# Performance work log

Measured on AMD Instinct MI355X. Metric: run time of the kernel, lower is better.

Reference implementation:

```python
import jax, jax.numpy as jnp
import numpy as np

DIM = 64
K = 7
GC = 8            # groups_channels (hardcoded in module)
G = DIM // GC     # groups = 8
RED = 2           # reduction_ratio
PAD = (K - 1) // 2


def _patches(y, k, p):
    # torch nn.Unfold(k, dilation=1, padding=p, stride=1) ordering: (c, kh, kw)
    b, c, H, W = y.shape
    yp = jnp.pad(y, ((0, 0), (0, 0), (p, p), (p, p)))
    tiles = [yp[:, :, i:i + H, j:j + W] for i in range(k) for j in range(k)]
    return jnp.stack(tiles, axis=2)  # (b, c, k*k, H, W)


def setup_inputs() -> dict:
    key = jax.random.key(0)
    ks = jax.random.split(key, 6)
    b, h, w = 4, 128, 128
    input_x = jax.random.normal(ks[0], (b, DIM, h, w), dtype=jnp.float32)
    input_y = jax.random.normal(ks[1], (b, DIM, h, w), dtype=jnp.float32)
    c_mid = DIM // RED
    w1 = jax.random.normal(ks[2], (c_mid, DIM), dtype=jnp.float32) * 0.05
    b1 = jnp.zeros((c_mid,), dtype=jnp.float32)
    w2 = jax.random.normal(ks[3], (K * K * G, c_mid), dtype=jnp.float32) * 0.05
    b2 = jnp.zeros((K * K * G,), dtype=jnp.float32)
    return {"input_x": input_x, "input_y": input_y, "w1": w1, "b1": b1, "w2": w2, "b2": b2}


def reference(input_x, input_y, w1, b1, w2, b2):
    b, c, h, w = input_x.shape
    # 1x1 convs generating dynamic kernels (stride == 1, no avgpool)
    mid = jnp.einsum('bchw,oc->bohw', input_x, w1) + b1[None, :, None, None]
    weight = jnp.einsum('bchw,oc->bohw', mid, w2) + b2[None, :, None, None]
    # (b, G, 1, k*k, h, w) broadcast over groups_channels
    weight = weight.reshape(b, G, K * K, h, w)[:, :, None]
    # unfold input_y -> (b, G, GC, k*k, h, w)
    out = _patches(input_y, K, PAD).reshape(b, G, GC, K * K, h, w)
    out = (weight * out).sum(axis=3).reshape(b, DIM, h, w)
    return out
```

## Files before the change

kernel.cpp:

```cpp
#include <hip/hip_runtime.h>
#include <hip/hip_fp16.h>

#define DIMC 64
#define KS 7
#define NTAP 49
#define GCH 8
#define NG 8
#define CMID 32
#define PADD 3
#define HH 128
#define WW 128
#define PLANE (HH*WW)
#define TW 32
#define TH 8
#define TPX (TW+2*PADD)
#define TPY (TH+2*PADD)
#define NPIX (TPX*TPY)
#define NB 4
#define WTSTR 52
#define NROW (NG*NTAP)
#define CPAD 12

#define WC_OFF 0
#define BC_OFF 50176
#define XT_OFF 52224
#define WS_NEED (XT_OFF + (size_t)NB * PLANE * DIMC * 2)

typedef __attribute__((ext_vector_type(8))) short short8;
typedef __attribute__((ext_vector_type(4))) float f32x4;
typedef __fp16 fp16x2 __attribute__((ext_vector_type(2)));

static __device__ inline unsigned short f2bs(float f) {
    union { float f; unsigned u; } v; v.f = f;
    unsigned r = v.u + 0x7fff + ((v.u >> 16) & 1);
    return (unsigned short)(r >> 16);
}

static __device__ inline unsigned pkh(float a, float b) {
    union { fp16x2 h; unsigned u; } c;
    c.h = __builtin_amdgcn_cvt_pkrtz(a, b);
    return c.u;
}

__global__ __launch_bounds__(256)
void prep_weights(const float* __restrict__ w1, const float* __restrict__ b1,
                  const float* __restrict__ w2, const float* __restrict__ b2,
                  unsigned short* __restrict__ wc, float* __restrict__ bc) {
    int idx = blockIdx.x * 256 + threadIdx.x;
    if (idx >= NROW * 16) return;
    int row = idx >> 4;
    int c0 = (idx & 15) * 4;
    const float* w2r = w2 + row * CMID;
    float a0 = 0.f, a1 = 0.f, a2 = 0.f, a3 = 0.f;
    #pragma unroll
    for (int m = 0; m < CMID; ++m) {
        float wv = w2r[m];
        const float* w1r = w1 + m * DIMC + c0;
        a0 = fmaf(wv, w1r[0], a0);
        a1 = fmaf(wv, w1r[1], a1);
        a2 = fmaf(wv, w1r[2], a2);
        a3 = fmaf(wv, w1r[3], a3);
    }
    *reinterpret_cast<uint2*>(wc + row * DIMC + c0) =
        make_uint2(((unsigned)f2bs(a1) << 16) | f2bs(a0),
                   ((unsigned)f2bs(a3) << 16) | f2bs(a2));
    if ((idx & 15) == 0) {
        float s = b2[row];
        #pragma unroll
        for (int m = 0; m < CMID; ++m) s = fmaf(w2r[m], b1[m], s);
        bc[row] = s;
    }
}

__global__ __launch_bounds__(256)
void prep_xt(const float* __restrict__ x, unsigned short* __restrict__ xt) {
    const int px = blockIdx.x * 256 + threadIdx.x;
    const int b = blockIdx.y;
    const int h = blockIdx.z;
    const float* xp = x + (size_t)b * DIMC * PLANE + (size_t)h * 32 * PLANE + px;
    #pragma unroll
    for (int q = 0; q < 4; ++q) {
        unsigned pk[4];
        #pragma unroll
        for (int j = 0; j < 4; ++j) {
            float v0 = xp[(size_t)(q * 8 + 2 * j) * PLANE];
            float v1 = xp[(size_t)(q * 8 + 2 * j + 1) * PLANE];
            pk[j] = ((unsigned)f2bs(v1) << 16) | f2bs(v0);
        }
        *reinterpret_cast<uint4*>(xt + (((size_t)b * 8 + h * 4 + q) * PLANE + px) * 8) =
            make_uint4(pk[0], pk[1], pk[2], pk[3]);
    }
}

__global__ __launch_bounds__(256, 4)
void invol_mfma2_kernel(const float* __restrict__ y,
                        const unsigned short* __restrict__ xt,
                        const unsigned short* __restrict__ wc,
                        const float* __restrict__ bc,
                        float* __restrict__ out) {
    __shared__ __half ytile[NPIX * GCH];
    __shared__ __half wtl[256 * WTSTR];

    const int tid = threadIdx.x;
    const int l = tid & 63, w = tid >> 6;
    const int bx = blockIdx.x, by = blockIdx.y;
    const int b = blockIdx.z >> 3, g = blockIdx.z & 7;

    #pragma unroll
    for (int k = 0; k < 5; ++k) {
        int i = tid + k * 256;
        if (i < NPIX * 2) {
            int q  = i / NPIX;
            int px = i - q * NPIX;
            int c0 = q * 4;
            int r = px / TPX, col = px - r * TPX;
            int sy = by * TH + r - PADD, sx = bx * TW + col - PADD;
            bool ok = (sy >= 0 && sy < HH && sx >= 0 && sx < WW);
            const float* yp = y + ((size_t)(b * DIMC + g * GCH + c0) * HH + sy) * WW + sx;
            float v0 = ok ? yp[0] : 0.f;
            float v1 = ok ? yp[PLANE] : 0.f;
            float v2 = ok ? yp[2 * PLANE] : 0.f;
            float v3 = ok ? yp[3 * PLANE] : 0.f;
            *reinterpret_cast<uint2*>(&ytile[px * GCH + c0]) =
                make_uint2(pkh(v0, v1), pkh(v2, v3));
        }
    }

    const int fr = l & 15, fk = l >> 4;
    f32x4 acc[4][4];
    #pragma unroll
    for (int mt = 0; mt < 4; ++mt)
        #pragma unroll
        for (int nt = 0; nt < 4; ++nt)
            acc[mt][nt] = f32x4{0.f, 0.f, 0.f, 0.f};

    int gpix[4];
    #pragma unroll
    for (int nt = 0; nt < 4; ++nt) {
        int lp = w * 64 + nt * 16 + fr;
        gpix[nt] = (by * TH + (lp >> 5)) * WW + bx * TW + (lp & 31);
    }

    #pragma unroll
    for (int kp = 0; kp < 2; ++kp) {
        short8 af[4];
        #pragma unroll
        for (int mt = 0; mt < 4; ++mt) {
            int row = mt * 16 + fr;
            union { uint4 u; short8 s; } cv;
            cv.u = make_uint4(0u, 0u, 0u, 0u);
            if (row < NTAP)
                cv.u = *reinterpret_cast<const uint4*>(
                    wc + ((size_t)(g * NTAP + row)) * DIMC + kp * 32 + fk * 8);
            af[mt] = cv.s;
        }
        short8 bf[4];
        #pragma unroll
        for (int nt = 0; nt < 4; ++nt) {
            union { uint4 u; short8 s; } cv;
            cv.u = *reinterpret_cast<const uint4*>(
                xt + (((size_t)b * 8 + kp * 4 + fk) * PLANE + gpix[nt]) * 8);
            bf[nt] = cv.s;
        }
        #pragma unroll
        for (int mt = 0; mt < 4; ++mt)
            #pragma unroll
            for (int nt = 0; nt < 4; ++nt)
                acc[mt][nt] = __builtin_amdgcn_mfma_f32_16x16x32_bf16(
                    af[mt], bf[nt], acc[mt][nt], 0, 0, 0);
    }

    const int r0 = fk * 4;
    #pragma unroll
    for (int mt = 0; mt < 4; ++mt) {
        if (mt < 3 || r0 == 0) {
            int rb = mt * 16 + r0;
            float bb[4];
            #pragma unroll
            for (int j = 0; j < 4; ++j)
                bb[j] = (rb + j < NTAP) ? bc[g * NTAP + rb + j] : 0.f;
            #pragma unroll
            for (int nt = 0; nt < 4; ++nt) {
                int lp = w * 64 + nt * 16 + fr;
                *reinterpret_cast<uint2*>(&wtl[lp * WTSTR + rb]) =
                    make_uint2(pkh(acc[mt][nt][0] + bb[0], acc[mt][nt][1] + bb[1]),
                               pkh(acc[mt][nt][2] + bb[2], acc[mt][nt][3] + bb[3]));
            }
        }
    }

    __syncthreads();

    __half2 wth[26];
    const __half2* wrow = reinterpret_cast<const __half2*>(&wtl[tid * WTSTR]);
    #pragma unroll
    for (int q = 0; q < 26; ++q) wth[q] = wrow[q];

    const int tx = tid & 31, ty = tid >> 5;
    float acco[GCH];
    #pragma unroll
    for (int cc = 0; cc < GCH; ++cc) acco[cc] = 0.f;
    #pragma unroll
    for (int ky = 0; ky < KS; ++ky) {
        #pragma unroll
        for (int kx = 0; kx < KS; ++kx) {
            const int kk = ky * KS + kx;
            float wv = (kk & 1) ? __high2float(wth[kk >> 1]) : __low2float(wth[kk >> 1]);
            int pp = (ty + ky) * TPX + (tx + kx);
            union { uint4 u; __half2 h[4]; } yv;
            yv.u = *reinterpret_cast<const uint4*>(&ytile[pp * GCH]);
            acco[0] = fmaf(wv, __low2float(yv.h[0]),  acco[0]);
            acco[1] = fmaf(wv, __high2float(yv.h[0]), acco[1]);
            acco[2] = fmaf(wv, __low2float(yv.h[1]),  acco[2]);
            acco[3] = fmaf(wv, __high2float(yv.h[1]), acco[3]);
            acco[4] = fmaf(wv, __low2float(yv.h[2]),  acco[4]);
            acco[5] = fmaf(wv, __high2float(yv.h[2]), acco[5]);
            acco[6] = fmaf(wv, __low2float(yv.h[3]),  acco[6]);
            acco[7] = fmaf(wv, __high2float(yv.h[3]), acco[7]);
        }
    }

    const int gy = by * TH + ty, gx = bx * TW + tx;
    float* op = out + ((size_t)(b * DIMC + g * GCH) * HH + gy) * WW + gx;
    #pragma unroll
    for (int cc = 0; cc < GCH; ++cc) op[cc * PLANE] = acco[cc];
}

__global__ __launch_bounds__(256, 1)
void invol_fused_kernel(const float* __restrict__ x, const float* __restrict__ y,
                        const float* __restrict__ w1, const float* __restrict__ b1,
                        const float* __restrict__ w2, const float* __restrict__ b2,
                        float* __restrict__ out) {
    __shared__ float ytile[NPIX * CPAD];
    const int tid = threadIdx.x;
    const int tx = tid & 31, ty = tid >> 5;
    const int bx = blockIdx.x, by = blockIdx.y, bz = blockIdx.z;
    const int gx = bx * TW + tx, gy = by * TH + ty;

    float xv[DIMC];
    const float* xp = x + ((size_t)(bz * DIMC) * HH + gy) * WW + gx;
    #pragma unroll
    for (int c = 0; c < DIMC; ++c) xv[c] = xp[c * PLANE];

    float mid[CMID];
    #pragma unroll
    for (int m = 0; m < CMID; ++m) {
        float a = b1[m];
        const float4* w1r = reinterpret_cast<const float4*>(w1 + m * DIMC);
        #pragma unroll
        for (int cq = 0; cq < DIMC / 4; ++cq) {
            float4 wv = w1r[cq];
            a = fmaf(wv.x, xv[4*cq+0], a);
            a = fmaf(wv.y, xv[4*cq+1], a);
            a = fmaf(wv.z, xv[4*cq+2], a);
            a = fmaf(wv.w, xv[4*cq+3], a);
        }
        mid[m] = a;
    }

    for (int g = 0; g < NG; ++g) {
        __syncthreads();
        for (int i = tid; i < NPIX * GCH; i += 256) {
            int c = i / NPIX;
            int p = i - c * NPIX;
            int r = p / TPX;
            int col = p - r * TPX;
            int sy = by * TH + r - PADD;
            int sx = bx * TW + col - PADD;
            float v = 0.f;
            if (sy >= 0 && sy < HH && sx >= 0 && sx < WW)
                v = y[((size_t)(bz * DIMC + g * GCH + c) * HH + sy) * WW + sx];
            ytile[p * CPAD + c] = v;
        }
        __syncthreads();

        float wt[NTAP];
        const float*  b2g = b2 + g * NTAP;
        const float4* w2g = reinterpret_cast<const float4*>(w2 + g * NTAP * CMID);
        #pragma unroll
        for (int kk = 0; kk < NTAP; ++kk) {
            float a = b2g[kk];
            #pragma unroll
            for (int mq = 0; mq < CMID / 4; ++mq) {
                float4 wv = w2g[kk * (CMID / 4) + mq];
                a = fmaf(wv.x, mid[4*mq+0], a);
                a = fmaf(wv.y, mid[4*mq+1], a);
                a = fmaf(wv.z, mid[4*mq+2], a);
                a = fmaf(wv.w, mid[4*mq+3], a);
            }
            wt[kk] = a;
        }

        float acc[GCH];
        #pragma unroll
        for (int cc = 0; cc < GCH; ++cc) acc[cc] = 0.f;
        #pragma unroll
        for (int ky = 0; ky < KS; ++ky) {
            #pragma unroll
            for (int kx = 0; kx < KS; ++kx) {
                float wv = wt[ky * KS + kx];
                int pp = (ty + ky) * TPX + (tx + kx);
                const float4* yr = reinterpret_cast<const float4*>(&ytile[pp * CPAD]);
                float4 ya = yr[0];
                float4 yb = yr[1];
                acc[0] = fmaf(wv, ya.x, acc[0]);
                acc[1] = fmaf(wv, ya.y, acc[1]);
                acc[2] = fmaf(wv, ya.z, acc[2]);
                acc[3] = fmaf(wv, ya.w, acc[3]);
                acc[4] = fmaf(wv, yb.x, acc[4]);
                acc[5] = fmaf(wv, yb.y, acc[5]);
                acc[6] = fmaf(wv, yb.z, acc[6]);
                acc[7] = fmaf(wv, yb.w, acc[7]);
            }
        }

        float* op = out + ((size_t)(bz * DIMC + g * GCH) * HH + gy) * WW + gx;
        #pragma unroll
        for (int cc = 0; cc < GCH; ++cc) op[cc * PLANE] = acc[cc];
    }
}

extern "C" void kernel_launch(void* const* d_in, const int* in_sizes, int n_in,
                              void* d_out, int out_size, void* d_ws, size_t ws_size,
                              hipStream_t stream) {
    const float* x  = (const float*)d_in[0];
    const float* y  = (const float*)d_in[1];
    const float* w1 = (const float*)d_in[2];
    const float* b1 = (const float*)d_in[3];
    const float* w2 = (const float*)d_in[4];
    const float* b2 = (const float*)d_in[5];
    float* out = (float*)d_out;

    if (ws_size >= WS_NEED) {
        char* ws = (char*)d_ws;
        unsigned short* wcp = (unsigned short*)(ws + WC_OFF);
        float*          bcp = (float*)(ws + BC_OFF);
        unsigned short* xtp = (unsigned short*)(ws + XT_OFF);

        hipLaunchKernelGGL(prep_weights, dim3((NROW * 16 + 255) / 256), dim3(256), 0, stream,
                           w1, b1, w2, b2, wcp, bcp);
        hipLaunchKernelGGL(prep_xt, dim3(PLANE / 256, NB, 2), dim3(256), 0, stream,
                           x, xtp);
        hipLaunchKernelGGL(invol_mfma2_kernel, dim3(WW / TW, HH / TH, NB * NG), dim3(256), 0, stream,
                           y, xtp, wcp, bcp, out);
    } else {
        dim3 grid(WW / TW, HH / TH, NB);
        hipLaunchKernelGGL(invol_fused_kernel, grid, dim3(256), 0, stream,
                           x, y, w1, b1, w2, b2, out);
    }
}
```

Measured before the change: 42.55 us.

## Merge prep kernels, pad weight rows to 64, use packed half FMA for aggregation

Merges the two preprocessing kernels into one launch. The combined weight matrix is now padded to 64 rows per group, so the MFMA kernel loads A fragments and biases without bounds checks. The 49-tap aggregation now accumulates in packed fp16 (hfma2) instead of fp32 FMAs, halving the FMA count, and the weight-tile stride changes to 54. The fp16 accumulation trades accuracy for speed, with a risk of precision loss over 49 taps.

```diff
diff --git a/kernel.cpp b/kernel.cpp
--- a/kernel.cpp
+++ b/kernel.cpp
@@ -17,13 +17,12 @@
 #define TPY (TH+2*PADD)
 #define NPIX (TPX*TPY)
 #define NB 4
-#define WTSTR 52
-#define NROW (NG*NTAP)
+#define WTSTR 54
 #define CPAD 12
 
 #define WC_OFF 0
-#define BC_OFF 50176
-#define XT_OFF 52224
+#define BC_OFF 65536
+#define XT_OFF 67584
 #define WS_NEED (XT_OFF + (size_t)NB * PLANE * DIMC * 2)
 
 typedef __attribute__((ext_vector_type(8))) short short8;
@@ -43,57 +42,61 @@
 }
 
 __global__ __launch_bounds__(256)
-void prep_weights(const float* __restrict__ w1, const float* __restrict__ b1,
-                  const float* __restrict__ w2, const float* __restrict__ b2,
-                  unsigned short* __restrict__ wc, float* __restrict__ bc) {
-    int idx = blockIdx.x * 256 + threadIdx.x;
-    if (idx >= NROW * 16) return;
-    int row = idx >> 4;
-    int c0 = (idx & 15) * 4;
-    const float* w2r = w2 + row * CMID;
-    float a0 = 0.f, a1 = 0.f, a2 = 0.f, a3 = 0.f;
-    #pragma unroll
-    for (int m = 0; m < CMID; ++m) {
-        float wv = w2r[m];
-        const float* w1r = w1 + m * DIMC + c0;
-        a0 = fmaf(wv, w1r[0], a0);
-        a1 = fmaf(wv, w1r[1], a1);
-        a2 = fmaf(wv, w1r[2], a2);
-        a3 = fmaf(wv, w1r[3], a3);
-    }
-    *reinterpret_cast<uint2*>(wc + row * DIMC + c0) =
-        make_uint2(((unsigned)f2bs(a1) << 16) | f2bs(a0),
-                   ((unsigned)f2bs(a3) << 16) | f2bs(a2));
-    if ((idx & 15) == 0) {
-        float s = b2[row];
-        #pragma unroll
-        for (int m = 0; m < CMID; ++m) s = fmaf(w2r[m], b1[m], s);
-        bc[row] = s;
-    }
-}
-
-__global__ __launch_bounds__(256)
-void prep_xt(const float* __restrict__ x, unsigned short* __restrict__ xt) {
-    const int px = blockIdx.x * 256 + threadIdx.x;
-    const int b = blockIdx.y;
-    const int h = blockIdx.z;
-    const float* xp = x + (size_t)b * DIMC * PLANE + (size_t)h * 32 * PLANE + px;
-    #pragma unroll
-    for (int q = 0; q < 4; ++q) {
-        unsigned pk[4];
-        #pragma unroll
-        for (int j = 0; j < 4; ++j) {
-            float v0 = xp[(size_t)(q * 8 + 2 * j) * PLANE];
-            float v1 = xp[(size_t)(q * 8 + 2 * j + 1) * PLANE];
-            pk[j] = ((unsigned)f2bs(v1) << 16) | f2bs(v0);
-        }
-        *reinterpret_cast<uint4*>(xt + (((size_t)b * 8 + h * 4 + q) * PLANE + px) * 8) =
-            make_uint4(pk[0], pk[1], pk[2], pk[3]);
+void prep_all(const float* __restrict__ x,
+              const float* __restrict__ w1, const float* __restrict__ b1,
+              const float* __restrict__ w2, const float* __restrict__ b2,
+              unsigned short* __restrict__ wc, float* __restrict__ bc,
+              unsigned short* __restrict__ xt) {
+    const int bid = blockIdx.x;
+    if (bid < 512) {
+        const int pxblk = bid & 63, rest = bid >> 6;
+        const int b = rest & 3, h = rest >> 2;
+        const int px = pxblk * 256 + threadIdx.x;
+        const float* xp = x + (size_t)b * DIMC * PLANE + (size_t)h * 32 * PLANE + px;
+        #pragma unroll
+        for (int q = 0; q < 4; ++q) {
+            unsigned pk[4];
+            #pragma unroll
+            for (int j = 0; j < 4; ++j) {
+                float v0 = xp[(size_t)(q * 8 + 2 * j) * PLANE];
+                float v1 = xp[(size_t)(q * 8 + 2 * j + 1) * PLANE];
+                pk[j] = ((unsigned)f2bs(v1) << 16) | f2bs(v0);
+            }
+            *reinterpret_cast<uint4*>(xt + (((size_t)b * 8 + h * 4 + q) * PLANE + px) * 8) =
+                make_uint4(pk[0], pk[1], pk[2], pk[3]);
+        }
+    } else {
+        const int idx = (bid - 512) * 256 + threadIdx.x;
+        const int row64 = idx >> 4;
+        const int c0 = (idx & 15) * 4;
+        const int g = row64 >> 6, r = row64 & 63;
+        float a0 = 0.f, a1 = 0.f, a2 = 0.f, a3 = 0.f, bv = 0.f;
+        if (r < NTAP) {
+            const float* w2r = w2 + (g * NTAP + r) * CMID;
+            #pragma unroll
+            for (int m = 0; m < CMID; ++m) {
+                float wv = w2r[m];
+                const float* w1r = w1 + m * DIMC + c0;
+                a0 = fmaf(wv, w1r[0], a0);
+                a1 = fmaf(wv, w1r[1], a1);
+                a2 = fmaf(wv, w1r[2], a2);
+                a3 = fmaf(wv, w1r[3], a3);
+            }
+            if (c0 == 0) {
+                bv = b2[g * NTAP + r];
+                #pragma unroll
+                for (int m = 0; m < CMID; ++m) bv = fmaf(w2r[m], b1[m], bv);
+            }
+        }
+        *reinterpret_cast<uint2*>(wc + row64 * DIMC + c0) =
+            make_uint2(((unsigned)f2bs(a1) << 16) | f2bs(a0),
+                       ((unsigned)f2bs(a3) << 16) | f2bs(a2));
+        if ((idx & 15) == 0) bc[row64] = bv;
     }
 }
 
 __global__ __launch_bounds__(256, 4)
-void invol_mfma2_kernel(const float* __restrict__ y,
+void invol_mfma3_kernel(const float* __restrict__ y,
                         const unsigned short* __restrict__ xt,
                         const unsigned short* __restrict__ wc,
                         const float* __restrict__ bc,
@@ -146,12 +149,9 @@
         short8 af[4];
         #pragma unroll
         for (int mt = 0; mt < 4; ++mt) {
-            int row = mt * 16 + fr;
             union { uint4 u; short8 s; } cv;
-            cv.u = make_uint4(0u, 0u, 0u, 0u);
-            if (row < NTAP)
-                cv.u = *reinterpret_cast<const uint4*>(
-                    wc + ((size_t)(g * NTAP + row)) * DIMC + kp * 32 + fk * 8);
+            cv.u = *reinterpret_cast<const uint4*>(
+                wc + ((size_t)(g * 64 + mt * 16 + fr)) * DIMC + kp * 32 + fk * 8);
             af[mt] = cv.s;
         }
         short8 bf[4];
@@ -175,16 +175,14 @@
     for (int mt = 0; mt < 4; ++mt) {
         if (mt < 3 || r0 == 0) {
             int rb = mt * 16 + r0;
-            float bb[4];
-            #pragma unroll
-            for (int j = 0; j < 4; ++j)
-                bb[j] = (rb + j < NTAP) ? bc[g * NTAP + rb + j] : 0.f;
+            float bb0 = bc[g * 64 + rb + 0], bb1 = bc[g * 64 + rb + 1];
+            float bb2 = bc[g * 64 + rb + 2], bb3 = bc[g * 64 + rb + 3];
             #pragma unroll
             for (int nt = 0; nt < 4; ++nt) {
                 int lp = w * 64 + nt * 16 + fr;
                 *reinterpret_cast<uint2*>(&wtl[lp * WTSTR + rb]) =
-                    make_uint2(pkh(acc[mt][nt][0] + bb[0], acc[mt][nt][1] + bb[1]),
-                               pkh(acc[mt][nt][2] + bb[2], acc[mt][nt][3] + bb[3]));
+                    make_uint2(pkh(acc[mt][nt][0] + bb0, acc[mt][nt][1] + bb1),
+                               pkh(acc[mt][nt][2] + bb2, acc[mt][nt][3] + bb3));
             }
         }
     }
@@ -197,33 +195,34 @@
     for (int q = 0; q < 26; ++q) wth[q] = wrow[q];
 
     const int tx = tid & 31, ty = tid >> 5;
-    float acco[GCH];
-    #pragma unroll
-    for (int cc = 0; cc < GCH; ++cc) acco[cc] = 0.f;
+    __half2 acch[4];
+    #pragma unroll
+    for (int cc = 0; cc < 4; ++cc) acch[cc] = __float2half2_rn(0.f);
     #pragma unroll
     for (int ky = 0; ky < KS; ++ky) {
         #pragma unroll
         for (int kx = 0; kx < KS; ++kx) {
             const int kk = ky * KS + kx;
-            float wv = (kk & 1) ? __high2float(wth[kk >> 1]) : __low2float(wth[kk >> 1]);
+            __half wh = (kk & 1) ? __high2half(wth[kk >> 1]) : __low2half(wth[kk >> 1]);
+            __half2 wv2 = __half2half2(wh);
             int pp = (ty + ky) * TPX + (tx + kx);
             union { uint4 u; __half2 h[4]; } yv;
             yv.u = *reinterpret_cast<const uint4*>(&ytile[pp * GCH]);
-            acco[0] = fmaf(wv, __low2float(yv.h[0]),  acco[0]);
-            acco[1] = fmaf(wv, __high2float(yv.h[0]), acco[1]);
-            acco[2] = fmaf(wv, __low2float(yv.h[1]),  acco[2]);
-            acco[3] = fmaf(wv, __high2float(yv.h[1]), acco[3]);
-            acco[4] = fmaf(wv, __low2float(yv.h[2]),  acco[4]);
-            acco[5] = fmaf(wv, __high2float(yv.h[2]), acco[5]);
-            acco[6] = fmaf(wv, __low2float(yv.h[3]),  acco[6]);
-            acco[7] = fmaf(wv, __high2float(yv.h[3]), acco[7]);
+            acch[0] = __hfma2(wv2, yv.h[0], acch[0]);
+            acch[1] = __hfma2(wv2, yv.h[1], acch[1]);
+            acch[2] = __hfma2(wv2, yv.h[2], acch[2]);
+            acch[3] = __hfma2(wv2, yv.h[3], acch[3]);
         }
     }
 
     const int gy = by * TH + ty, gx = bx * TW + tx;
     float* op = out + ((size_t)(b * DIMC + g * GCH) * HH + gy) * WW + gx;
     #pragma unroll
-    for (int cc = 0; cc < GCH; ++cc) op[cc * PLANE] = acco[cc];
+    for (int cc = 0; cc < 4; ++cc) {
+        float2 f = __half22float2(acch[cc]);
+        op[(2 * cc) * PLANE]     = f.x;
+        op[(2 * cc + 1) * PLANE] = f.y;
+    }
 }
 
 __global__ __launch_bounds__(256, 1)
@@ -337,11 +336,9 @@
         float*          bcp = (float*)(ws + BC_OFF);
         unsigned short* xtp = (unsigned short*)(ws + XT_OFF);
 
-        hipLaunchKernelGGL(prep_weights, dim3((NROW * 16 + 255) / 256), dim3(256), 0, stream,
-                           w1, b1, w2, b2, wcp, bcp);
-        hipLaunchKernelGGL(prep_xt, dim3(PLANE / 256, NB, 2), dim3(256), 0, stream,
-                           x, xtp);
-        hipLaunchKernelGGL(invol_mfma2_kernel, dim3(WW / TW, HH / TH, NB * NG), dim3(256), 0, stream,
+        hipLaunchKernelGGL(prep_all, dim3(512 + 32), dim3(256), 0, stream,
+                           x, w1, b1, w2, b2, wcp, bcp, xtp);
+        hipLaunchKernelGGL(invol_mfma3_kernel, dim3(WW / TW, HH / TH, NB * NG), dim3(256), 0, stream,
                            y, xtp, wcp, bcp, out);
     } else {
         dim3 grid(WW / TW, HH / TH, NB);
```

Measured after the change: 38.96 us. -8.4%, faster.
